# Kernel optimization log

Hardware: AMD Instinct MI355X
Metric: run time of the kernel (lower is better)

Reference implementation:

```python
import jax, jax.numpy as jnp
import numpy as np

B, T, C = 8, 1024, 384
L, H, D, F = 8, 16, 24, 1536
EPS = 1e-5

def _ln(x, g, b):
    m = jnp.mean(x, axis=-1, keepdims=True)
    v = jnp.mean(jnp.square(x - m), axis=-1, keepdims=True)
    return (x - m) * jax.lax.rsqrt(v + EPS) * g + b

def setup_inputs() -> dict:
    key = jax.random.key(0)
    ks = jax.random.split(key, 8)
    s = 0.02
    return {
        "idx": jax.random.uniform(ks[0], (B, T, C), jnp.float32),
        "pos_emb": jax.random.normal(ks[1], (T, C), jnp.float32) * s,
        "Wq": jax.random.normal(ks[2], (L, H, C, D), jnp.float32) * s,
        "Wk": jax.random.normal(ks[3], (L, H, C, D), jnp.float32) * s,
        "Wv": jax.random.normal(ks[4], (L, H, C, D), jnp.float32) * s,
        "Wo": jax.random.normal(ks[5], (L, C, C), jnp.float32) * s,
        "bo": jnp.zeros((L, C), jnp.float32),
        "ln1_g": jnp.ones((L, C), jnp.float32),
        "ln1_b": jnp.zeros((L, C), jnp.float32),
        "ln2_g": jnp.ones((L, C), jnp.float32),
        "ln2_b": jnp.zeros((L, C), jnp.float32),
        "W1": jax.random.normal(ks[6], (L, C, F), jnp.float32) * s,
        "b1": jnp.zeros((L, F), jnp.float32),
        "W2": jax.random.normal(ks[7], (L, F, C), jnp.float32) * s,
        "b2": jnp.zeros((L, C), jnp.float32),
        "lnf_g": jnp.ones((C,), jnp.float32),
        "lnf_b": jnp.zeros((C,), jnp.float32),
    }

def reference(idx, pos_emb, Wq, Wk, Wv, Wo, bo, ln1_g, ln1_b, ln2_g, ln2_b,
              W1, b1, W2, b2, lnf_g, lnf_b):
    Bc, Tc, Cc = idx.shape
    x = idx + pos_emb[:Tc]
    causal = jnp.tril(jnp.ones((Tc, Tc), bool))  # [T,T]
    scale = D ** -0.5
    for l in range(L):
        h = _ln(x, ln1_g[l], ln1_b[l])
        q = jnp.einsum('btc,hcd->bhtd', h, Wq[l])
        k = jnp.einsum('btc,hcd->bhtd', h, Wk[l])
        v = jnp.einsum('btc,hcd->bhtd', h, Wv[l])
        wei = jnp.einsum('bhtd,bhsd->bhts', q, k) * scale
        wei = jnp.where(causal, wei, -jnp.inf)
        wei = jax.nn.softmax(wei, axis=-1)
        o = jnp.einsum('bhts,bhsd->bhtd', wei, v)
        o = o.transpose(0, 2, 1, 3).reshape(Bc, Tc, H * D)
        x = x + o @ Wo[l] + bo[l]
        h2 = _ln(x, ln2_g[l], ln2_b[l])
        x = x + jax.nn.relu(h2 @ W1[l] + b1[l]) @ W2[l] + b2[l]
    x = _ln(x, lnf_g, lnf_b)
    return jax.nn.relu(x)  # MSE path with targets=None
```

## Files before the change

kernel.cpp:

```cpp
#include <hip/hip_runtime.h>

#define B_ 8
#define T_ 1024
#define C_ 384
#define L_ 8
#define H_ 16
#define D_ 24
#define F_ 1536
#define M_ 8192

using bf16x8 = __attribute__((ext_vector_type(8))) __bf16;
using f32x4  = __attribute__((ext_vector_type(4))) float;

__device__ __forceinline__ ushort f2b(float f) {
  union { float f; unsigned u; } cv; cv.f = f;
  unsigned u = cv.u;
  return (ushort)((u + 0x7FFFu + ((u >> 16) & 1u)) >> 16);
}
__device__ __forceinline__ ushort f2b_cvt(float f) {
  __bf16 h = (__bf16)f;
  return *(ushort*)&h;
}
__device__ __forceinline__ void gload_lds16(const void* g, void* l) {
  __builtin_amdgcn_global_load_lds((const __attribute__((address_space(1))) void*)g,
                                   (__attribute__((address_space(3))) void*)l, 16, 0, 0);
}

__global__ __launch_bounds__(256) void k_embed(const float* __restrict__ idx,
                                               const float* __restrict__ pos,
                                               float* __restrict__ x) {
  long i4 = ((long)blockIdx.x * 256 + threadIdx.x) * 4;
  float4 a = *(const float4*)(idx + i4);
  long p = i4 % (long)(T_ * C_);
  float4 b = *(const float4*)(pos + p);
  a.x += b.x; a.y += b.y; a.z += b.z; a.w += b.w;
  *(float4*)(x + i4) = a;
}

__global__ __launch_bounds__(256) void k_ln(const float* __restrict__ x,
                                            const float* __restrict__ g,
                                            const float* __restrict__ b,
                                            ushort* __restrict__ out) {
  int row  = blockIdx.x * 4 + (threadIdx.x >> 6);
  int lane = threadIdx.x & 63;
  const float* xr = x + (long)row * C_;
  float v[6]; float sum = 0.f;
#pragma unroll
  for (int i = 0; i < 3; ++i) {
    float2 t = *(const float2*)(xr + 2*(lane + 64*i));
    v[2*i] = t.x; v[2*i+1] = t.y; sum += t.x + t.y;
  }
#pragma unroll
  for (int m = 1; m < 64; m <<= 1) sum += __shfl_xor(sum, m);
  float mean = sum * (1.f / C_);
  float vs = 0.f;
#pragma unroll
  for (int i = 0; i < 6; ++i) { float d = v[i] - mean; vs += d * d; }
#pragma unroll
  for (int m = 1; m < 64; m <<= 1) vs += __shfl_xor(vs, m);
  float rstd = rsqrtf(vs * (1.f / C_) + 1e-5f);
  ushort* orow = out + (long)row * C_;
#pragma unroll
  for (int i = 0; i < 3; ++i) {
    int c = 2*(lane + 64*i);
    float2 gg = *(const float2*)(g + c);
    float2 bb = *(const float2*)(b + c);
    ushort2 w;
    w.x = f2b((v[2*i]   - mean) * rstd * gg.x + bb.x);
    w.y = f2b((v[2*i+1] - mean) * rstd * gg.y + bb.y);
    *(ushort2*)(orow + c) = w;
  }
}

__global__ __launch_bounds__(256) void k_lnf(const float* __restrict__ x,
                                             const float* __restrict__ g,
                                             const float* __restrict__ b,
                                             float* __restrict__ out) {
  int row  = blockIdx.x * 4 + (threadIdx.x >> 6);
  int lane = threadIdx.x & 63;
  const float* xr = x + (long)row * C_;
  float v[6]; float sum = 0.f;
#pragma unroll
  for (int i = 0; i < 3; ++i) {
    float2 t = *(const float2*)(xr + 2*(lane + 64*i));
    v[2*i] = t.x; v[2*i+1] = t.y; sum += t.x + t.y;
  }
#pragma unroll
  for (int m = 1; m < 64; m <<= 1) sum += __shfl_xor(sum, m);
  float mean = sum * (1.f / C_);
  float vs = 0.f;
#pragma unroll
  for (int i = 0; i < 6; ++i) { float d = v[i] - mean; vs += d * d; }
#pragma unroll
  for (int m = 1; m < 64; m <<= 1) vs += __shfl_xor(vs, m);
  float rstd = rsqrtf(vs * (1.f / C_) + 1e-5f);
  float* orow = out + (long)row * C_;
#pragma unroll
  for (int i = 0; i < 3; ++i) {
    int c = 2*(lane + 64*i);
    float2 gg = *(const float2*)(g + c);
    float2 bb = *(const float2*)(b + c);
    float2 w;
    w.x = fmaxf((v[2*i]   - mean) * rstd * gg.x + bb.x, 0.f);
    w.y = fmaxf((v[2*i+1] - mean) * rstd * gg.y + bb.y, 0.f);
    *(float2*)(orow + c) = w;
  }
}

__global__ __launch_bounds__(256) void k_trans_qkv(const float* __restrict__ src,
                                                   ushort* __restrict__ dst, int which) {
  __shared__ float tile[32][33];
  int z = blockIdx.z;
  int l = z >> 4, hh = z & 15;
  const float* sb = src + (long)z * C_ * D_;
  ushort* db = dst + (long)l * (3*C_) * C_ + (long)(which * C_ + hh * D_) * C_;
  int r0 = blockIdx.y * 32;
  int tx = threadIdx.x & 31, ty = threadIdx.x >> 5;
#pragma unroll
  for (int i = 0; i < 32; i += 8)
    tile[ty + i][tx] = (tx < D_) ? sb[(long)(r0 + ty + i) * D_ + tx] : 0.f;
  __syncthreads();
#pragma unroll
  for (int i = 0; i < 32; i += 8) {
    int s = ty + i, r = r0 + tx;
    if (s < D_) db[(long)s * C_ + r] = f2b(tile[tx][ty + i]);
  }
}

__global__ __launch_bounds__(256) void k_trans_w(const float* __restrict__ src,
                                                 ushort* __restrict__ dst, int R, int S) {
  __shared__ float tile[32][33];
  const float* sb = src + (long)blockIdx.z * R * S;
  ushort* db = dst + (long)blockIdx.z * R * S;
  int r0 = blockIdx.y * 32, s0 = blockIdx.x * 32;
  int tx = threadIdx.x & 31, ty = threadIdx.x >> 5;
#pragma unroll
  for (int i = 0; i < 32; i += 8) {
    int r = r0 + ty + i, s = s0 + tx;
    tile[ty + i][tx] = (r < R && s < S) ? sb[(long)r * S + s] : 0.f;
  }
  __syncthreads();
#pragma unroll
  for (int i = 0; i < 32; i += 8) {
    int s = s0 + ty + i, r = r0 + tx;
    if (s < S && r < R) db[(long)s * R + r] = f2b(tile[tx][ty + i]);
  }
}

template<int BN>
__global__ __launch_bounds__(256) void k_gemm(const ushort* __restrict__ A, int lda,
                                              const ushort* __restrict__ Bt, int ldb,
                                              const float* __restrict__ bias,
                                              const float* resid,
                                              float* outF, ushort* outB,
                                              ushort* qp, ushort* kp, ushort* vt,
                                              int N, int K, int relu) {
  __shared__ ushort As[128 * 64];
  __shared__ ushort Bs[BN * 64];
  constexpr int ITB = BN / 32;
  constexpr int MF  = (BN == 128) ? 4 : 2;
  int m0 = blockIdx.y * 128, n0 = blockIdx.x * BN;
  int tid = threadIdx.x, lane = tid & 63, wid = tid >> 6;
  int wr = (BN == 128) ? (wid >> 1) * 64 : wid * 32;
  int wc = (BN == 128) ? (wid & 1) * 64 : 0;
  int g = lane >> 4, q = lane & 15;
  f32x4 acc[MF][4] = {};

  for (int k0 = 0; k0 < K; k0 += 64) {
    __syncthreads();
#pragma unroll
    for (int it = 0; it < 4; ++it) {
      int idx = tid + it * 256;
      int r = idx >> 3;
      int ch = ((idx & 7) ^ (r & 7)) << 3;
      gload_lds16(A + (long)(m0 + r) * lda + k0 + ch,
                  (char*)As + (wid * 64 + it * 256) * 16);
    }
#pragma unroll
    for (int it = 0; it < ITB; ++it) {
      int idx = tid + it * 256;
      int r = idx >> 3;
      int ch = ((idx & 7) ^ (r & 7)) << 3;
      gload_lds16(Bt + (long)(n0 + r) * ldb + k0 + ch,
                  (char*)Bs + (wid * 64 + it * 256) * 16);
    }
    __syncthreads();
#pragma unroll
    for (int kk = 0; kk < 2; ++kk) {
      bf16x8 af[MF], bfr[4];
#pragma unroll
      for (int mi = 0; mi < MF; ++mi) {
        int row = wr + mi * 16 + q;
        int byt = ((row * 64 + kk * 32 + g * 8) * 2) ^ ((row & 7) << 4);
        af[mi] = *(const bf16x8*)((const char*)As + byt);
      }
#pragma unroll
      for (int ni = 0; ni < 4; ++ni) {
        int row = wc + ni * 16 + q;
        int byt = ((row * 64 + kk * 32 + g * 8) * 2) ^ ((row & 7) << 4);
        bfr[ni] = *(const bf16x8*)((const char*)Bs + byt);
      }
#pragma unroll
      for (int mi = 0; mi < MF; ++mi)
#pragma unroll
        for (int ni = 0; ni < 4; ++ni)
          acc[mi][ni] = __builtin_amdgcn_mfma_f32_16x16x32_bf16(af[mi], bfr[ni], acc[mi][ni], 0, 0, 0);
    }
  }
#pragma unroll
  for (int mi = 0; mi < MF; ++mi)
#pragma unroll
    for (int ni = 0; ni < 4; ++ni) {
      int rb = m0 + wr + mi * 16 + g * 4;
      int cc = n0 + wc + ni * 16 + q;
      float bv = bias ? bias[cc] : 0.f;
      float vals[4];
#pragma unroll
      for (int j = 0; j < 4; ++j) {
        float val = acc[mi][ni][j] + bv;
        if (resid) val += resid[(long)(rb + j) * N + cc];
        if (relu)  val = fmaxf(val, 0.f);
        vals[j] = val;
      }
      if (qp) {
        int sec = (cc >= 768) ? 2 : ((cc >= 384) ? 1 : 0);
        int col = cc - sec * 384;
        int hd = (col * 43691) >> 20;
        int dd = col - hd * 24;
        int bb = rb >> 10, tt = rb & 1023;
        int bh = bb * 16 + hd;
        if (sec == 2) {
          ushort4 w4 = { f2b(vals[0]), f2b(vals[1]), f2b(vals[2]), f2b(vals[3]) };
          *(ushort4*)(vt + ((long)bh * 32 + dd) * 1024 + tt) = w4;
        } else {
          ushort* dst = (sec ? kp : qp) + ((long)bh * 1024 + tt) * 32 + dd;
#pragma unroll
          for (int j = 0; j < 4; ++j) dst[j * 32] = f2b(vals[j]);
        }
      } else {
#pragma unroll
        for (int j = 0; j < 4; ++j) {
          long off = (long)(rb + j) * N + cc;
          if (outF) outF[off] = vals[j];
          if (outB) outB[off] = f2b(vals[j]);
        }
      }
    }
}

__global__ __launch_bounds__(256) void k_attn(const ushort* __restrict__ Qp,
                                              const ushort* __restrict__ Kp,
                                              const ushort* __restrict__ Vt,
                                              ushort* __restrict__ o) {
  __shared__ ushort Ps[4][16][136];
  int bh = blockIdx.x, t0 = blockIdx.y * 64;
  int b = bh >> 4, hh = bh & 15;
  int tid = threadIdx.x, lane = tid & 63, w = tid >> 6;
  int g = lane >> 4, q = lane & 15;
  const float scale = 0.20412414523193154f;
  const f32x4 zf = {0.f, 0.f, 0.f, 0.f};

  const ushort* qb  = Qp + (long)bh * 1024 * 32;
  const ushort* kb_ = Kp + (long)bh * 1024 * 32;
  const ushort* vtb = Vt + (long)bh * 32 * 1024;
  bf16x8 qa = *(const bf16x8*)(qb + (t0 + w * 16 + q) * 32 + g * 8);

  f32x4 acc0 = zf, acc1 = zf;
  float lsum[4] = {0.f, 0.f, 0.f, 0.f};
  int send = t0 + 64;

  for (int s0 = 0; s0 < send; s0 += 128) {
    int rem = send - s0;
    int siMax = (rem >= 128) ? 8 : (rem >> 4);
    int kkMax = (rem >= 128) ? 4 : (rem >> 5);
    f32x4 sc[8];
#pragma unroll
    for (int si = 0; si < 8; ++si) {
      if (si < siMax) {
        bf16x8 kb = *(const bf16x8*)(kb_ + (s0 + si * 16 + q) * 32 + g * 8);
        sc[si] = __builtin_amdgcn_mfma_f32_16x16x32_bf16(qa, kb, zf, 0, 0, 0);
      }
    }
#pragma unroll
    for (int si = 0; si < 8; ++si) {
      if (si < siMax) {
        int s_abs = s0 + si * 16 + q;
#pragma unroll
        for (int j = 0; j < 4; ++j) {
          int t_abs = t0 + w * 16 + g * 4 + j;
          float p = (s_abs <= t_abs) ? __expf(sc[si][j] * scale) : 0.f;
          lsum[j] += p;
          Ps[w][g * 4 + j][si * 16 + q] = f2b_cvt(p);
        }
      }
    }
#pragma unroll
    for (int kk = 0; kk < 4; ++kk) {
      if (kk < kkMax) {
        bf16x8 pa  = *(const bf16x8*)(&Ps[w][q][kk * 32 + g * 8]);
        bf16x8 vb0 = *(const bf16x8*)(vtb + (long)q * 1024 + s0 + kk * 32 + g * 8);
        acc0 = __builtin_amdgcn_mfma_f32_16x16x32_bf16(pa, vb0, acc0, 0, 0, 0);
        bf16x8 vb1 = *(const bf16x8*)(vtb + (long)(16 + q) * 1024 + s0 + kk * 32 + g * 8);
        acc1 = __builtin_amdgcn_mfma_f32_16x16x32_bf16(pa, vb1, acc1, 0, 0, 0);
      }
    }
  }
#pragma unroll
  for (int m = 1; m < 16; m <<= 1)
#pragma unroll
    for (int j = 0; j < 4; ++j) lsum[j] += __shfl_xor(lsum[j], m);
#pragma unroll
  for (int j = 0; j < 4; ++j) {
    float inv = 1.f / lsum[j];
    int t_abs = t0 + w * 16 + g * 4 + j;
    long orow = (long)(b * T_ + t_abs) * C_ + hh * D_;
    o[orow + q] = f2b(acc0[j] * inv);
    if (q < 8) o[orow + 16 + q] = f2b(acc1[j] * inv);
  }
}

extern "C" void kernel_launch(void* const* d_in, const int* in_sizes, int n_in,
                              void* d_out, int out_size, void* d_ws, size_t ws_size,
                              hipStream_t stream) {
  (void)in_sizes; (void)n_in; (void)out_size; (void)ws_size;
  const float* idx  = (const float*)d_in[0];
  const float* pos  = (const float*)d_in[1];
  const float* Wq   = (const float*)d_in[2];
  const float* Wk   = (const float*)d_in[3];
  const float* Wv   = (const float*)d_in[4];
  const float* Wo   = (const float*)d_in[5];
  const float* bo   = (const float*)d_in[6];
  const float* ln1g = (const float*)d_in[7];
  const float* ln1b = (const float*)d_in[8];
  const float* ln2g = (const float*)d_in[9];
  const float* ln2b = (const float*)d_in[10];
  const float* W1   = (const float*)d_in[11];
  const float* b1   = (const float*)d_in[12];
  const float* W2   = (const float*)d_in[13];
  const float* b2   = (const float*)d_in[14];
  const float* lnfg = (const float*)d_in[15];
  const float* lnfb = (const float*)d_in[16];

  char* ws = (char*)d_ws;
  float*  x     = (float*)(ws);
  ushort* h     = (ushort*)(ws + 12582912);
  ushort* Qp    = (ushort*)(ws + 18874368);
  ushort* Kp    = (ushort*)(ws + 27262976);
  ushort* Vt    = (ushort*)(ws + 35651584);
  ushort* u     = (ushort*)(ws + 44040192);
  ushort* WqkvT = (ushort*)(ws + 69206016);
  ushort* WoT   = (ushort*)(ws + 76283904);
  ushort* W1T   = (ushort*)(ws + 78643200);
  ushort* W2T   = (ushort*)(ws + 88080384);

  hipMemsetAsync(Qp, 0, 25165824, stream);

  k_trans_qkv<<<dim3(1, 12, L_ * H_), 256, 0, stream>>>(Wq, WqkvT, 0);
  k_trans_qkv<<<dim3(1, 12, L_ * H_), 256, 0, stream>>>(Wk, WqkvT, 1);
  k_trans_qkv<<<dim3(1, 12, L_ * H_), 256, 0, stream>>>(Wv, WqkvT, 2);
  k_trans_w<<<dim3(12, 12, L_), 256, 0, stream>>>(Wo, WoT, C_, C_);
  k_trans_w<<<dim3(48, 12, L_), 256, 0, stream>>>(W1, W1T, C_, F_);
  k_trans_w<<<dim3(12, 48, L_), 256, 0, stream>>>(W2, W2T, F_, C_);

  k_embed<<<(M_ * C_) / (256 * 4), 256, 0, stream>>>(idx, pos, x);

  for (int l = 0; l < L_; ++l) {
    k_ln<<<M_ / 4, 256, 0, stream>>>(x, ln1g + l * C_, ln1b + l * C_, h);
    k_gemm<128><<<dim3(1152 / 128, M_ / 128), 256, 0, stream>>>(
        h, C_, WqkvT + (long)l * 1152 * C_, C_,
        nullptr, nullptr, nullptr, nullptr, Qp, Kp, Vt, 1152, C_, 0);
    k_attn<<<dim3(B_ * H_, T_ / 64), 256, 0, stream>>>(Qp, Kp, Vt, h);
    k_gemm<64><<<dim3(C_ / 64, M_ / 128), 256, 0, stream>>>(
        h, C_, WoT + (long)l * C_ * C_, C_,
        bo + l * C_, x, x, nullptr, nullptr, nullptr, nullptr, C_, C_, 0);
    k_ln<<<M_ / 4, 256, 0, stream>>>(x, ln2g + l * C_, ln2b + l * C_, h);
    k_gemm<128><<<dim3(F_ / 128, M_ / 128), 256, 0, stream>>>(
        h, C_, W1T + (long)l * F_ * C_, C_,
        b1 + l * F_, nullptr, nullptr, u, nullptr, nullptr, nullptr, F_, C_, 1);
    k_gemm<64><<<dim3(C_ / 64, M_ / 128), 256, 0, stream>>>(
        u, F_, W2T + (long)l * C_ * F_, F_,
        b2 + l * C_, x, x, nullptr, nullptr, nullptr, nullptr, C_, F_, 0);
  }
  k_lnf<<<M_ / 4, 256, 0, stream>>>(x, lnfg, lnfb, (float*)d_out);
}
```

Before: 1.563 ms.

## Fold softmax scale into Q, compute row sums via ones column, balance causal attention blocks

Q is pre-scaled by scale*log2(e) in the QKV GEMM epilogue so attention uses exp2f with no per-element multiply. A constant column of ones is written into padded V row 24, so the P·V MFMA also produces the softmax denominator and the shuffle reduction of lsum goes away. Each attention block now handles two query tiles (by and 15-by) to balance the causal workload, halving the grid, and K fragments are prefetched one tile ahead. Without max-subtraction the exp can overflow for large scores, which relies on small activations.

```diff
diff --git a/kernel.cpp b/kernel.cpp
--- a/kernel.cpp
+++ b/kernel.cpp
@@ -25,6 +25,8 @@
   __builtin_amdgcn_global_load_lds((const __attribute__((address_space(1))) void*)g,
                                    (__attribute__((address_space(3))) void*)l, 16, 0, 0);
 }
+
+#define QSCL 0.29448870f
 
 __global__ __launch_bounds__(256) void k_embed(const float* __restrict__ idx,
                                                const float* __restrict__ pos,
@@ -145,6 +147,11 @@
     int s = s0 + ty + i, r = r0 + tx;
     if (s < S && r < R) db[(long)s * R + r] = f2b(tile[tx][ty + i]);
   }
+}
+
+__global__ __launch_bounds__(256) void k_ones(ushort* __restrict__ Vt) {
+  ushort4 one4 = {0x3F80, 0x3F80, 0x3F80, 0x3F80};
+  *(ushort4*)(Vt + ((long)blockIdx.x * 32 + 24) * 1024 + threadIdx.x * 4) = one4;
 }
 
 template<int BN>
@@ -233,9 +240,10 @@
           ushort4 w4 = { f2b(vals[0]), f2b(vals[1]), f2b(vals[2]), f2b(vals[3]) };
           *(ushort4*)(vt + ((long)bh * 32 + dd) * 1024 + tt) = w4;
         } else {
+          float sfac = sec ? 1.f : QSCL;
           ushort* dst = (sec ? kp : qp) + ((long)bh * 1024 + tt) * 32 + dd;
 #pragma unroll
-          for (int j = 0; j < 4; ++j) dst[j * 32] = f2b(vals[j]);
+          for (int j = 0; j < 4; ++j) dst[j * 32] = f2b(vals[j] * sfac);
         }
       } else {
 #pragma unroll
@@ -253,50 +261,46 @@
                                               const ushort* __restrict__ Vt,
                                               ushort* __restrict__ o) {
   __shared__ ushort Ps[4][16][136];
-  int bh = blockIdx.x, t0 = blockIdx.y * 64;
+  int bh = blockIdx.x, by = blockIdx.y;
   int b = bh >> 4, hh = bh & 15;
   int tid = threadIdx.x, lane = tid & 63, w = tid >> 6;
   int g = lane >> 4, q = lane & 15;
-  const float scale = 0.20412414523193154f;
   const f32x4 zf = {0.f, 0.f, 0.f, 0.f};
 
   const ushort* qb  = Qp + (long)bh * 1024 * 32;
   const ushort* kb_ = Kp + (long)bh * 1024 * 32;
   const ushort* vtb = Vt + (long)bh * 32 * 1024;
-  bf16x8 qa = *(const bf16x8*)(qb + (t0 + w * 16 + q) * 32 + g * 8);
-
-  f32x4 acc0 = zf, acc1 = zf;
-  float lsum[4] = {0.f, 0.f, 0.f, 0.f};
-  int send = t0 + 64;
-
-  for (int s0 = 0; s0 < send; s0 += 128) {
-    int rem = send - s0;
-    int siMax = (rem >= 128) ? 8 : (rem >> 4);
-    int kkMax = (rem >= 128) ? 4 : (rem >> 5);
-    f32x4 sc[8];
-#pragma unroll
-    for (int si = 0; si < 8; ++si) {
-      if (si < siMax) {
-        bf16x8 kb = *(const bf16x8*)(kb_ + (s0 + si * 16 + q) * 32 + g * 8);
-        sc[si] = __builtin_amdgcn_mfma_f32_16x16x32_bf16(qa, kb, zf, 0, 0, 0);
-      }
-    }
-#pragma unroll
-    for (int si = 0; si < 8; ++si) {
-      if (si < siMax) {
-        int s_abs = s0 + si * 16 + q;
-#pragma unroll
-        for (int j = 0; j < 4; ++j) {
-          int t_abs = t0 + w * 16 + g * 4 + j;
-          float p = (s_abs <= t_abs) ? __expf(sc[si][j] * scale) : 0.f;
-          lsum[j] += p;
-          Ps[w][g * 4 + j][si * 16 + q] = f2b_cvt(p);
-        }
-      }
-    }
-#pragma unroll
-    for (int kk = 0; kk < 4; ++kk) {
-      if (kk < kkMax) {
+
+#pragma unroll
+  for (int pass = 0; pass < 2; ++pass) {
+    int t0 = (pass ? (15 - by) : by) * 64;
+    int send = t0 + 64;
+    int nT = (send + 127) >> 7;
+
+    bf16x8 qa = *(const bf16x8*)(qb + (t0 + w * 16 + q) * 32 + g * 8);
+    f32x4 acc0 = zf, acc1 = zf;
+
+    bf16x8 kf[8];
+#pragma unroll
+    for (int si = 0; si < 8; ++si)
+      kf[si] = *(const bf16x8*)(kb_ + (si * 16 + q) * 32 + g * 8);
+
+    for (int it = 0; it < nT - 1; ++it) {
+      int s0 = it << 7;
+      f32x4 sc[8];
+#pragma unroll
+      for (int si = 0; si < 8; ++si)
+        sc[si] = __builtin_amdgcn_mfma_f32_16x16x32_bf16(qa, kf[si], zf, 0, 0, 0);
+#pragma unroll
+      for (int si = 0; si < 8; ++si)
+        kf[si] = *(const bf16x8*)(kb_ + (s0 + 128 + si * 16 + q) * 32 + g * 8);
+#pragma unroll
+      for (int si = 0; si < 8; ++si)
+#pragma unroll
+        for (int j = 0; j < 4; ++j)
+          Ps[w][g * 4 + j][si * 16 + q] = f2b_cvt(exp2f(sc[si][j]));
+#pragma unroll
+      for (int kk = 0; kk < 4; ++kk) {
         bf16x8 pa  = *(const bf16x8*)(&Ps[w][q][kk * 32 + g * 8]);
         bf16x8 vb0 = *(const bf16x8*)(vtb + (long)q * 1024 + s0 + kk * 32 + g * 8);
         acc0 = __builtin_amdgcn_mfma_f32_16x16x32_bf16(pa, vb0, acc0, 0, 0, 0);
@@ -304,18 +308,46 @@
         acc1 = __builtin_amdgcn_mfma_f32_16x16x32_bf16(pa, vb1, acc1, 0, 0, 0);
       }
     }
-  }
-#pragma unroll
-  for (int m = 1; m < 16; m <<= 1)
-#pragma unroll
-    for (int j = 0; j < 4; ++j) lsum[j] += __shfl_xor(lsum[j], m);
-#pragma unroll
-  for (int j = 0; j < 4; ++j) {
-    float inv = 1.f / lsum[j];
-    int t_abs = t0 + w * 16 + g * 4 + j;
-    long orow = (long)(b * T_ + t_abs) * C_ + hh * D_;
-    o[orow + q] = f2b(acc0[j] * inv);
-    if (q < 8) o[orow + 16 + q] = f2b(acc1[j] * inv);
+    {
+      int s0 = (nT - 1) << 7;
+      int rem = send - s0;
+      int siMax = rem >> 4, kkMax = rem >> 5;
+      f32x4 sc[8];
+#pragma unroll
+      for (int si = 0; si < 8; ++si)
+        if (si < siMax)
+          sc[si] = __builtin_amdgcn_mfma_f32_16x16x32_bf16(qa, kf[si], zf, 0, 0, 0);
+#pragma unroll
+      for (int si = 0; si < 8; ++si)
+        if (si < siMax) {
+          int s_abs = s0 + si * 16 + q;
+#pragma unroll
+          for (int j = 0; j < 4; ++j) {
+            int t_abs = t0 + w * 16 + g * 4 + j;
+            float p = (s_abs <= t_abs) ? exp2f(sc[si][j]) : 0.f;
+            Ps[w][g * 4 + j][si * 16 + q] = f2b_cvt(p);
+          }
+        }
+#pragma unroll
+      for (int kk = 0; kk < 4; ++kk)
+        if (kk < kkMax) {
+          bf16x8 pa  = *(const bf16x8*)(&Ps[w][q][kk * 32 + g * 8]);
+          bf16x8 vb0 = *(const bf16x8*)(vtb + (long)q * 1024 + s0 + kk * 32 + g * 8);
+          acc0 = __builtin_amdgcn_mfma_f32_16x16x32_bf16(pa, vb0, acc0, 0, 0, 0);
+          bf16x8 vb1 = *(const bf16x8*)(vtb + (long)(16 + q) * 1024 + s0 + kk * 32 + g * 8);
+          acc1 = __builtin_amdgcn_mfma_f32_16x16x32_bf16(pa, vb1, acc1, 0, 0, 0);
+        }
+    }
+    int src = (lane & 48) | 8;
+#pragma unroll
+    for (int j = 0; j < 4; ++j) {
+      float ls = __shfl(acc1[j], src);
+      float iv = 1.f / ls;
+      int t_abs = t0 + w * 16 + g * 4 + j;
+      long orow = (long)(b * T_ + t_abs) * C_ + hh * D_;
+      o[orow + q] = f2b(acc0[j] * iv);
+      if (q < 8) o[orow + 16 + q] = f2b(acc1[j] * iv);
+    }
   }
 }
 
@@ -354,6 +386,7 @@
   ushort* W2T   = (ushort*)(ws + 88080384);
 
   hipMemsetAsync(Qp, 0, 25165824, stream);
+  k_ones<<<128, 256, 0, stream>>>(Vt);
 
   k_trans_qkv<<<dim3(1, 12, L_ * H_), 256, 0, stream>>>(Wq, WqkvT, 0);
   k_trans_qkv<<<dim3(1, 12, L_ * H_), 256, 0, stream>>>(Wk, WqkvT, 1);
@@ -369,7 +402,7 @@
     k_gemm<128><<<dim3(1152 / 128, M_ / 128), 256, 0, stream>>>(
         h, C_, WqkvT + (long)l * 1152 * C_, C_,
         nullptr, nullptr, nullptr, nullptr, Qp, Kp, Vt, 1152, C_, 0);
-    k_attn<<<dim3(B_ * H_, T_ / 64), 256, 0, stream>>>(Qp, Kp, Vt, h);
+    k_attn<<<dim3(B_ * H_, 8), 256, 0, stream>>>(Qp, Kp, Vt, h);
     k_gemm<64><<<dim3(C_ / 64, M_ / 128), 256, 0, stream>>>(
         h, C_, WoT + (long)l * C_ * C_, C_,
         bo + l * C_, x, x, nullptr, nullptr, nullptr, nullptr, C_, C_, 0);
```

New measurement: 1.572 ms. Within noise of the previous version (+0.5%).
